# Performance work log

Measured on AMD Instinct MI355X. Metric: run time of the kernel, lower is better.

The kernel has to match this reference:

```python
import jax, jax.numpy as jnp
import numpy as np

LAYER_NORM_EPS = 1e-6
N_HEAD, D_MODEL, D_HEAD = 16, 1024, 64
QLEN, RLEN, BSZ = 2048, 2048, 2


def _rel_shift(x):
    # x: [T, C, b, n] -> Transformer-XL relative shift
    T, C = x.shape[0], x.shape[1]
    tail = x.shape[2:]
    zero_pad = jnp.zeros((T, 1) + tail, dtype=x.dtype)
    x_padded = jnp.concatenate([zero_pad, x], axis=1)          # [T, C+1, b, n]
    x_padded = x_padded.reshape((C + 1, T) + tail)             # [C+1, T, b, n]
    return x_padded[1:].reshape(x.shape)                       # [T, C, b, n]


def _layer_norm(x, gamma, beta):
    mu = jnp.mean(x, axis=-1, keepdims=True)
    var = jnp.mean(jnp.square(x - mu), axis=-1, keepdims=True)
    return (x - mu) * jax.lax.rsqrt(var + LAYER_NORM_EPS) * gamma + beta


def setup_inputs() -> dict:
    key = jax.random.key(0)
    ks = jax.random.split(key, 8)
    s_qkv = 1.0 / np.sqrt(D_MODEL)
    return {
        "h": jax.random.normal(ks[0], (QLEN, BSZ, D_MODEL), jnp.float32),
        "r": jax.random.normal(ks[1], (RLEN, D_MODEL), jnp.float32),
        "r_w_bias": jax.random.normal(ks[2], (N_HEAD, D_HEAD), jnp.float32) * 0.02,
        "r_r_bias": jax.random.normal(ks[3], (N_HEAD, D_HEAD), jnp.float32) * 0.02,
        "W_qkv": jax.random.normal(ks[4], (D_MODEL, 3 * N_HEAD * D_HEAD), jnp.float32) * s_qkv,
        "W_r": jax.random.normal(ks[5], (D_MODEL, N_HEAD * D_HEAD), jnp.float32) * s_qkv,
        "W_o": jax.random.normal(ks[6], (N_HEAD * D_HEAD, D_MODEL), jnp.float32) * s_qkv,
        "ln_gamma": jnp.ones((D_MODEL,), jnp.float32),
        "ln_beta": jnp.zeros((D_MODEL,), jnp.float32),
    }


def reference(h, r, r_w_bias, r_r_bias, W_qkv, W_r, W_o, ln_gamma, ln_beta):
    qlen, bsz = h.shape[0], h.shape[1]
    n_head, d_head = N_HEAD, D_HEAD
    scale = 1.0 / np.sqrt(d_head).astype(np.float32)

    w_heads = h @ W_qkv                                   # [q, b, 3*n*d]
    w_q, w_k, w_v = jnp.split(w_heads, 3, axis=-1)
    r_k = (r @ W_r).reshape(r.shape[0], n_head, d_head)    # [rlen, n, d]

    klen = w_k.shape[0]
    w_q = w_q.reshape(qlen, bsz, n_head, d_head)
    w_k = w_k.reshape(klen, bsz, n_head, d_head)
    w_v = w_v.reshape(klen, bsz, n_head, d_head)

    AC = jnp.einsum('ibnd,jbnd->ijbn', w_q + r_w_bias, w_k)
    BD = jnp.einsum('ibnd,jnd->ijbn', w_q + r_r_bias, r_k)
    BD = _rel_shift(BD)

    attn_score = (AC + BD) * scale                         # [q, k, b, n]
    attn_prob = jax.nn.softmax(attn_score, axis=1)

    attn_vec = jnp.einsum('ijbn,jbnd->ibnd', attn_prob, w_v)
    attn_vec = attn_vec.reshape(qlen, bsz, n_head * d_head)
    attn_out = attn_vec @ W_o                              # [q, b, d_model]

    # post-norm residual (pre_norm=False)
    return _layer_norm(h + attn_out, ln_gamma, ln_beta)
```

## Files before the change

### kernel.cpp

```cpp
#include <hip/hip_runtime.h>
#include <hip/hip_bf16.h>

typedef unsigned short u16;
typedef __attribute__((ext_vector_type(8))) short s16x8;
typedef __attribute__((ext_vector_type(8))) unsigned short u16x8;
typedef __attribute__((ext_vector_type(4))) float f32x4;

#define SEQ 2048
#define KEXP 0.18033688011112042f

__device__ __forceinline__ float bf2f(u16 x) {
  union { unsigned u; float f; } c; c.u = ((unsigned)x) << 16; return c.f;
}
__device__ __forceinline__ u16 f2bf(float f) {
  __hip_bfloat16 h = __float2bfloat16(f);
  return __builtin_bit_cast(u16, h);
}
__device__ __forceinline__ unsigned pack2(float a, float b) {
  return (unsigned)f2bf(a) | ((unsigned)f2bf(b) << 16);
}

__global__ __launch_bounds__(256) void k_cvt(const float* __restrict__ src,
                                             u16* __restrict__ dst, int n4) {
  int i = blockIdx.x * 256 + threadIdx.x;
  if (i >= n4) return;
  float4 v = ((const float4*)src)[i];
  ((ushort4*)dst)[i] = make_ushort4(f2bf(v.x), f2bf(v.y), f2bf(v.z), f2bf(v.w));
}

__global__ __launch_bounds__(256) void k_tcvt(const float* __restrict__ src,
                                              u16* __restrict__ dst, int R, int C) {
  __shared__ u16 T[64][72];
  int r0 = blockIdx.y * 64, c0 = blockIdx.x * 64;
  int tid = threadIdx.x;
#pragma unroll
  for (int p = 0; p < 4; ++p) {
    int f = p * 256 + tid;
    int r = f >> 4, cc = (f & 15) * 4;
    float4 v = *(const float4*)(src + (size_t)(r0 + r) * C + c0 + cc);
    T[r][cc + 0] = f2bf(v.x); T[r][cc + 1] = f2bf(v.y);
    T[r][cc + 2] = f2bf(v.z); T[r][cc + 3] = f2bf(v.w);
  }
  __syncthreads();
#pragma unroll
  for (int p = 0; p < 2; ++p) {
    int f = p * 256 + tid;
    int c = f >> 3, rr = (f & 7) * 8;
    u16x8 v;
#pragma unroll
    for (int e = 0; e < 8; ++e) v[e] = T[rr + e][c];
    *(u16x8*)(dst + (size_t)(c0 + c) * R + r0 + rr) = v;
  }
}

template <int RES>
__global__ __launch_bounds__(256) void k_gemm_bt(const u16* __restrict__ A,
                                                 const u16* __restrict__ Bt,
                                                 u16* __restrict__ Cb,
                                                 float* __restrict__ Cf,
                                                 const float* __restrict__ res,
                                                 int M, int N, int K) {
  __shared__ u16 As[128 * 72];
  __shared__ u16 Bs[128 * 72];
  const int tid = threadIdx.x;
  const int l = tid & 63, wv = tid >> 6;
  const int g = l >> 4, c16 = l & 15;
  const int m0 = blockIdx.x * 128, n0 = blockIdx.y * 128;
  const int wr = (wv >> 1) * 64, wc = (wv & 1) * 64;
  f32x4 acc[4][4] = {};
  for (int k0 = 0; k0 < K; k0 += 64) {
    __syncthreads();
#pragma unroll
    for (int p = 0; p < 4; ++p) {
      int f = p * 256 + tid;
      int row = f >> 3, kb = (f & 7) * 8;
      u16x8 va = *(const u16x8*)(A + (size_t)(m0 + row) * K + k0 + kb);
      u16x8 vb = *(const u16x8*)(Bt + (size_t)(n0 + row) * K + k0 + kb);
      *(u16x8*)&As[row * 72 + kb] = va;
      *(u16x8*)&Bs[row * 72 + kb] = vb;
    }
    __syncthreads();
#pragma unroll
    for (int ks = 0; ks < 2; ++ks) {
      s16x8 af[4], bf[4];
#pragma unroll
      for (int fr = 0; fr < 4; ++fr)
        af[fr] = *(const s16x8*)&As[(wr + fr * 16 + c16) * 72 + ks * 32 + g * 8];
#pragma unroll
      for (int fc = 0; fc < 4; ++fc)
        bf[fc] = *(const s16x8*)&Bs[(wc + fc * 16 + c16) * 72 + ks * 32 + g * 8];
#pragma unroll
      for (int fr = 0; fr < 4; ++fr)
#pragma unroll
        for (int fc = 0; fc < 4; ++fc)
          acc[fr][fc] = __builtin_amdgcn_mfma_f32_16x16x32_bf16(af[fr], bf[fc],
                                                                acc[fr][fc], 0, 0, 0);
    }
  }
#pragma unroll
  for (int fr = 0; fr < 4; ++fr)
#pragma unroll
    for (int fc = 0; fc < 4; ++fc)
#pragma unroll
      for (int reg = 0; reg < 4; ++reg) {
        int row = m0 + wr + fr * 16 + g * 4 + reg;
        int col = n0 + wc + fc * 16 + c16;
        float v = acc[fr][fc][reg];
        if (RES) Cf[(size_t)row * N + col] = v + res[(size_t)row * N + col];
        else     Cb[(size_t)row * N + col] = f2bf(v);
      }
}

__global__ __launch_bounds__(256) void k_vt(const u16* __restrict__ qkv,
                                            u16* __restrict__ vT) {
  __shared__ u16 T[64][72];
  const int tid = threadIdx.x;
  const int j0 = blockIdx.x * 64;
  const int n = blockIdx.y & 15, b = blockIdx.y >> 4;
#pragma unroll
  for (int p = 0; p < 2; ++p) {
    int f = p * 256 + tid;
    int r = f >> 3, cc = (f & 7) * 8;
    *(u16x8*)&T[r][cc] =
        *(const u16x8*)(qkv + ((size_t)((j0 + r) * 2 + b)) * 3072 + 2048 + n * 64 + cc);
  }
  __syncthreads();
#pragma unroll
  for (int p = 0; p < 2; ++p) {
    int f = p * 256 + tid;
    int d = f >> 3, jc = (f & 7) * 8;
    u16x8 v;
#pragma unroll
    for (int e = 0; e < 8; ++e) v[e] = T[jc + e][d];
    *(u16x8*)(vT + ((size_t)((b * 16 + n) * 64 + d)) * 2048 + j0 + jc) = v;
  }
}

__global__ __launch_bounds__(256) void k_attn(const u16* __restrict__ qkv,
                                              const u16* __restrict__ rk,
                                              const u16* __restrict__ vT,
                                              const float* __restrict__ rwb,
                                              const float* __restrict__ rrb,
                                              u16* __restrict__ av) {
  __shared__ u16 Kt[128][72];
  __shared__ u16 Vt[64][136];
  __shared__ u16 St[192][66];
  __shared__ u16 Pt[64][136];

  const int tid = threadIdx.x;
  const int l = tid & 63, wv = tid >> 6;
  const int g = l >> 4, c16 = l & 15;
  const int s = blockIdx.x;
  const int y = (s & 7) + 8 * (s >> 8);
  const int x = (s >> 3) & 31;
  const int i0 = x * 64;
  const int n = y & 15, b = y >> 4;
  const f32x4 zero4 = {0.f, 0.f, 0.f, 0.f};
  const s16x8 zero8 = {0, 0, 0, 0, 0, 0, 0, 0};

  s16x8 qw[2];
  {
    int i = i0 + wv * 16 + c16;
    const u16* src = qkv + ((size_t)(i * 2 + b)) * 3072 + n * 64;
#pragma unroll
    for (int ks = 0; ks < 2; ++ks) {
      int d0 = ks * 32 + g * 8;
      u16x8 raw = *(const u16x8*)(src + d0);
      u16x8 wq;
#pragma unroll
      for (int e = 0; e < 8; ++e)
        wq[e] = f2bf(bf2f(raw[e]) + rwb[n * 64 + d0 + e]);
      qw[ks] = __builtin_bit_cast(s16x8, wq);
    }
  }
  s16x8 qr_a[4][2];
#pragma unroll
  for (int rg = 0; rg < 4; ++rg) {
    int i = i0 + rg * 16 + c16;
    const u16* src = qkv + ((size_t)(i * 2 + b)) * 3072 + n * 64;
#pragma unroll
    for (int ks = 0; ks < 2; ++ks) {
      int d0 = ks * 32 + g * 8;
      u16x8 raw = *(const u16x8*)(src + d0);
      u16x8 wq;
#pragma unroll
      for (int e = 0; e < 8; ++e)
        wq[e] = f2bf(bf2f(raw[e]) + rrb[n * 64 + d0 + e]);
      qr_a[rg][ks] = __builtin_bit_cast(s16x8, wq);
    }
  }
  s16x8 q64[2];
  {
    bool valid = (c16 == 0) && (i0 + 64 < SEQ);
#pragma unroll
    for (int ks = 0; ks < 2; ++ks) q64[ks] = zero8;
    if (valid) {
      const u16* src = qkv + ((size_t)((i0 + 64) * 2 + b)) * 3072 + n * 64;
#pragma unroll
      for (int ks = 0; ks < 2; ++ks) {
        int d0 = ks * 32 + g * 8;
        u16x8 raw = *(const u16x8*)(src + d0);
        u16x8 wq;
#pragma unroll
        for (int e = 0; e < 8; ++e)
          wq[e] = f2bf(bf2f(raw[e]) + rrb[n * 64 + d0 + e]);
        q64[ks] = __builtin_bit_cast(s16x8, wq);
      }
    }
  }

  u16x8 kpre[4], vpre[4];
  s16x8 rpre[3][2];
  auto issue_loads = [&](int j0n) {
#pragma unroll
    for (int p = 0; p < 4; ++p) {
      int f = p * 256 + tid;
      kpre[p] = *(const u16x8*)(qkv + ((size_t)((j0n + (f >> 3)) * 2 + b)) * 3072 +
                                1024 + n * 64 + (f & 7) * 8);
    }
#pragma unroll
    for (int p = 0; p < 4; ++p) {
      int f = p * 256 + tid;
      vpre[p] = *(const u16x8*)(vT + ((size_t)((b * 16 + n) * 64 + (f >> 4))) * 2048 +
                                j0n + (f & 15) * 8);
    }
#pragma unroll
    for (int c3 = 0; c3 < 3; ++c3) {
      int w = (wv * 3 + c3) * 16 + c16;
      int u = j0n - i0 - 63 + w;
      int c = (u <= 0) ? (u + (SEQ - 1)) : (u - 2);
      const u16* p = rk + (size_t)(c < 0 ? 0 : c) * 1024 + n * 64;
      rpre[c3][0] = *(const s16x8*)(p + g * 8);
      rpre[c3][1] = *(const s16x8*)(p + 32 + g * 8);
      if (c < 0) { rpre[c3][0] = zero8; rpre[c3][1] = zero8; }
    }
  };

  float m_prev[4], l_sum[4];
  f32x4 o_acc[4];
#pragma unroll
  for (int r = 0; r < 4; ++r) { m_prev[r] = -1e30f; l_sum[r] = 0.f; o_acc[r] = zero4; }

  issue_loads(0);

  for (int it = 0; it < 16; ++it) {
    const int j0 = it * 128;
    const int cfthr = (64 + i0 - j0) >> 4;
    __syncthreads();

#pragma unroll
    for (int p = 0; p < 4; ++p) {
      int f = p * 256 + tid;
      *(u16x8*)&Kt[f >> 3][(f & 7) * 8] = kpre[p];
    }
#pragma unroll
    for (int p = 0; p < 4; ++p) {
      int f = p * 256 + tid;
      *(u16x8*)&Vt[f >> 4][(f & 15) * 8] = vpre[p];
    }

#pragma unroll
    for (int c3 = 0; c3 < 3; ++c3) {
      const int cfe = wv * 3 + c3;
      const bool du = (cfe >= cfthr);
      const int w = cfe * 16 + c16;
#pragma unroll
      for (int rg = 0; rg < 4; ++rg) {
        f32x4 qr = zero4;
        qr = __builtin_amdgcn_mfma_f32_16x16x32_bf16(qr_a[rg][0], rpre[c3][0], qr, 0, 0, 0);
        qr = __builtin_amdgcn_mfma_f32_16x16x32_bf16(qr_a[rg][1], rpre[c3][1], qr, 0, 0, 0);
        const int B = rg * 16 + g * 4;
        if (!du) {
          *(unsigned*)&St[w][B] = pack2(qr[0], qr[1]);
          *(unsigned*)&St[w][B + 2] = pack2(qr[2], qr[3]);
        } else if (B == 0) {
          *(unsigned*)&St[w][0] = pack2(qr[1], qr[2]);
          St[w][2] = f2bf(qr[3]);
        } else {
          St[w][B - 1] = f2bf(qr[0]);
          *(unsigned*)&St[w][B] = pack2(qr[1], qr[2]);
          St[w][B + 2] = f2bf(qr[3]);
        }
      }
      if (du) {
        f32x4 q64o = zero4;
        q64o = __builtin_amdgcn_mfma_f32_16x16x32_bf16(q64[0], rpre[c3][0], q64o, 0, 0, 0);
        q64o = __builtin_amdgcn_mfma_f32_16x16x32_bf16(q64[1], rpre[c3][1], q64o, 0, 0, 0);
        if (g == 0) St[w][63] = f2bf(q64o[0]);
      }
    }
    __syncthreads();

    f32x4 sc[8];
#pragma unroll
    for (int fj = 0; fj < 8; ++fj) sc[fj] = zero4;
#pragma unroll
    for (int ks = 0; ks < 2; ++ks)
#pragma unroll
      for (int fj = 0; fj < 8; ++fj) {
        s16x8 bf = *(const s16x8*)&Kt[fj * 16 + c16][ks * 32 + g * 8];
        sc[fj] = __builtin_amdgcn_mfma_f32_16x16x32_bf16(qw[ks], bf, sc[fj], 0, 0, 0);
      }

    {
      const char* Sbase = (const char*)&St[0][0] +
                          (c16 * 132 - (wv * 16 + g * 4) * 130 + 7926);
#pragma unroll
      for (int fj = 0; fj < 8; ++fj)
#pragma unroll
        for (int reg = 0; reg < 4; ++reg)
          sc[fj][reg] += bf2f(*(const u16*)(Sbase + fj * 2112 + (3 - reg) * 130));
    }

    float mt[4];
#pragma unroll
    for (int reg = 0; reg < 4; ++reg) {
      mt[reg] = sc[0][reg];
#pragma unroll
      for (int fj = 1; fj < 8; ++fj) mt[reg] = fmaxf(mt[reg], sc[fj][reg]);
    }
#pragma unroll
    for (int off = 1; off < 16; off <<= 1)
#pragma unroll
      for (int reg = 0; reg < 4; ++reg)
        mt[reg] = fmaxf(mt[reg], __shfl_xor(mt[reg], off, 16));
    float al[4], rs[4];
#pragma unroll
    for (int reg = 0; reg < 4; ++reg) {
      float mn = fmaxf(m_prev[reg], mt[reg]);
      al[reg] = __builtin_amdgcn_exp2f((m_prev[reg] - mn) * KEXP);
      m_prev[reg] = mn;
      rs[reg] = 0.f;
    }
#pragma unroll
    for (int fj = 0; fj < 8; ++fj)
#pragma unroll
      for (int reg = 0; reg < 4; ++reg) {
        float p = __builtin_amdgcn_exp2f((sc[fj][reg] - m_prev[reg]) * KEXP);
        rs[reg] += p;
        Pt[wv * 16 + g * 4 + reg][fj * 16 + c16] = f2bf(p);
      }
#pragma unroll
    for (int off = 1; off < 16; off <<= 1)
#pragma unroll
      for (int reg = 0; reg < 4; ++reg)
        rs[reg] += __shfl_xor(rs[reg], off, 16);
#pragma unroll
    for (int reg = 0; reg < 4; ++reg)
      l_sum[reg] = l_sum[reg] * al[reg] + rs[reg];
#pragma unroll
    for (int fd = 0; fd < 4; ++fd)
#pragma unroll
      for (int reg = 0; reg < 4; ++reg)
        o_acc[fd][reg] *= al[reg];

    if (it < 15) issue_loads(j0 + 128);

#pragma unroll
    for (int ks = 0; ks < 4; ++ks) {
      s16x8 pa = *(const s16x8*)&Pt[wv * 16 + c16][ks * 32 + g * 8];
#pragma unroll
      for (int fd = 0; fd < 4; ++fd) {
        s16x8 vb = *(const s16x8*)&Vt[fd * 16 + c16][ks * 32 + g * 8];
        o_acc[fd] = __builtin_amdgcn_mfma_f32_16x16x32_bf16(pa, vb, o_acc[fd], 0, 0, 0);
      }
    }
  }

#pragma unroll
  for (int reg = 0; reg < 4; ++reg) {
    float inv = 1.0f / l_sum[reg];
    int i = i0 + wv * 16 + g * 4 + reg;
    u16* dst = av + ((size_t)(i * 2 + b)) * 1024 + n * 64;
#pragma unroll
    for (int fd = 0; fd < 4; ++fd)
      dst[fd * 16 + c16] = f2bf(o_acc[fd][reg] * inv);
  }
}

__global__ __launch_bounds__(256) void k_ln(const float* __restrict__ tmp,
                                            const float* __restrict__ gamma,
                                            const float* __restrict__ beta,
                                            float* __restrict__ out) {
  __shared__ float r1[4], r2[4];
  const int row = blockIdx.x, tid = threadIdx.x;
  const float* x = tmp + (size_t)row * 1024;
  float4 v = *(const float4*)(x + tid * 4);
  float s1 = v.x + v.y + v.z + v.w;
  float s2 = v.x * v.x + v.y * v.y + v.z * v.z + v.w * v.w;
#pragma unroll
  for (int off = 1; off < 64; off <<= 1) {
    s1 += __shfl_xor(s1, off, 64);
    s2 += __shfl_xor(s2, off, 64);
  }
  if ((tid & 63) == 0) { r1[tid >> 6] = s1; r2[tid >> 6] = s2; }
  __syncthreads();
  s1 = r1[0] + r1[1] + r1[2] + r1[3];
  s2 = r2[0] + r2[1] + r2[2] + r2[3];
  float mu = s1 * (1.f / 1024.f);
  float var = s2 * (1.f / 1024.f) - mu * mu;
  float rstd = rsqrtf(var + 1e-6f);
  float4 gm = *(const float4*)(gamma + tid * 4);
  float4 bt = *(const float4*)(beta + tid * 4);
  float4 o;
  o.x = (v.x - mu) * rstd * gm.x + bt.x;
  o.y = (v.y - mu) * rstd * gm.y + bt.y;
  o.z = (v.z - mu) * rstd * gm.z + bt.z;
  o.w = (v.w - mu) * rstd * gm.w + bt.w;
  *(float4*)(out + (size_t)row * 1024 + tid * 4) = o;
}

extern "C" void kernel_launch(void* const* d_in, const int* in_sizes, int n_in,
                              void* d_out, int out_size, void* d_ws, size_t ws_size,
                              hipStream_t stream) {
  const float* h    = (const float*)d_in[0];
  const float* r    = (const float*)d_in[1];
  const float* rwb  = (const float*)d_in[2];
  const float* rrb  = (const float*)d_in[3];
  const float* Wqkv = (const float*)d_in[4];
  const float* Wr   = (const float*)d_in[5];
  const float* Wo   = (const float*)d_in[6];
  const float* gam  = (const float*)d_in[7];
  const float* bet  = (const float*)d_in[8];
  float* out = (float*)d_out;

  u16* hb     = (u16*)d_ws;
  u16* Wqkv_t = hb + (size_t)4096 * 1024;
  u16* Wr_t   = Wqkv_t + (size_t)3072 * 1024;
  u16* Wo_t   = Wr_t + (size_t)1024 * 1024;
  u16* rb     = Wo_t + (size_t)1024 * 1024;
  u16* qkv    = rb + (size_t)2048 * 1024;
  u16* rk     = qkv + (size_t)4096 * 3072;
  u16* vT     = rk + (size_t)2048 * 1024;
  u16* av     = vT + (size_t)2 * 16 * 64 * 2048;
  float* tmp  = (float*)(av + (size_t)4096 * 1024);

  k_cvt<<<4096, 256, 0, stream>>>(h, hb, 4096 * 1024 / 4);
  k_cvt<<<2048, 256, 0, stream>>>(r, rb, 2048 * 1024 / 4);
  k_tcvt<<<dim3(48, 16), 256, 0, stream>>>(Wqkv, Wqkv_t, 1024, 3072);
  k_tcvt<<<dim3(16, 16), 256, 0, stream>>>(Wr, Wr_t, 1024, 1024);
  k_tcvt<<<dim3(16, 16), 256, 0, stream>>>(Wo, Wo_t, 1024, 1024);
  k_gemm_bt<0><<<dim3(32, 24), 256, 0, stream>>>(hb, Wqkv_t, qkv, nullptr, nullptr,
                                                 4096, 3072, 1024);
  k_gemm_bt<0><<<dim3(16, 8), 256, 0, stream>>>(rb, Wr_t, rk, nullptr, nullptr,
                                                2048, 1024, 1024);
  k_vt<<<dim3(32, 32), 256, 0, stream>>>(qkv, vT);
  k_attn<<<1024, 256, 0, stream>>>(qkv, rk, vT, rwb, rrb, av);
  k_gemm_bt<1><<<dim3(32, 8), 256, 0, stream>>>(av, Wo_t, nullptr, tmp, h,
                                                4096, 1024, 1024);
  k_ln<<<4096, 256, 0, stream>>>(tmp, gam, bet, out);
}
```

Before: 279.3 us.

## Transpose attention score MFMA so softmax reductions stay per-lane

```diff
diff --git a/kernel.cpp b/kernel.cpp
--- a/kernel.cpp
+++ b/kernel.cpp
@@ -144,8 +144,8 @@
                                               u16* __restrict__ av) {
   __shared__ u16 Kt[128][72];
   __shared__ u16 Vt[64][136];
-  __shared__ u16 St[192][66];
-  __shared__ u16 Pt[64][136];
+  __shared__ u16 St2[64 * 200];
+  __shared__ u16 Pt[4][16][136];
 
   const int tid = threadIdx.x;
   const int l = tid & 63, wv = tid >> 6;
@@ -155,6 +155,7 @@
   const int x = (s >> 3) & 31;
   const int i0 = x * 64;
   const int n = y & 15, b = y >> 4;
+  const int ii = wv * 16 + c16;
   const f32x4 zero4 = {0.f, 0.f, 0.f, 0.f};
   const s16x8 zero8 = {0, 0, 0, 0, 0, 0, 0, 0};
 
@@ -173,29 +174,14 @@
       qw[ks] = __builtin_bit_cast(s16x8, wq);
     }
   }
-  s16x8 qr_a[4][2];
-#pragma unroll
-  for (int rg = 0; rg < 4; ++rg) {
-    int i = i0 + rg * 16 + c16;
-    const u16* src = qkv + ((size_t)(i * 2 + b)) * 3072 + n * 64;
-#pragma unroll
-    for (int ks = 0; ks < 2; ++ks) {
-      int d0 = ks * 32 + g * 8;
-      u16x8 raw = *(const u16x8*)(src + d0);
-      u16x8 wq;
-#pragma unroll
-      for (int e = 0; e < 8; ++e)
-        wq[e] = f2bf(bf2f(raw[e]) + rrb[n * 64 + d0 + e]);
-      qr_a[rg][ks] = __builtin_bit_cast(s16x8, wq);
-    }
-  }
-  s16x8 q64[2];
-  {
-    bool valid = (c16 == 0) && (i0 + 64 < SEQ);
-#pragma unroll
-    for (int ks = 0; ks < 2; ++ks) q64[ks] = zero8;
-    if (valid) {
-      const u16* src = qkv + ((size_t)((i0 + 64) * 2 + b)) * 3072 + n * 64;
+  s16x8 qr_b[4][2], qr_b1[4][2];
+#pragma unroll
+  for (int rb = 0; rb < 4; ++rb) {
+#pragma unroll
+    for (int sh = 0; sh < 2; ++sh) {
+      int i = i0 + rb * 16 + c16 + sh;
+      if (i > SEQ - 1) i = SEQ - 1;
+      const u16* src = qkv + ((size_t)(i * 2 + b)) * 3072 + n * 64;
 #pragma unroll
       for (int ks = 0; ks < 2; ++ks) {
         int d0 = ks * 32 + g * 8;
@@ -204,7 +190,8 @@
 #pragma unroll
         for (int e = 0; e < 8; ++e)
           wq[e] = f2bf(bf2f(raw[e]) + rrb[n * 64 + d0 + e]);
-        q64[ks] = __builtin_bit_cast(s16x8, wq);
+        if (sh == 0) qr_b[rb][ks] = __builtin_bit_cast(s16x8, wq);
+        else         qr_b1[rb][ks] = __builtin_bit_cast(s16x8, wq);
       }
     }
   }
@@ -236,16 +223,16 @@
     }
   };
 
-  float m_prev[4], l_sum[4];
+  float m_prev = -1e30f, l_sum = 0.f;
   f32x4 o_acc[4];
 #pragma unroll
-  for (int r = 0; r < 4; ++r) { m_prev[r] = -1e30f; l_sum[r] = 0.f; o_acc[r] = zero4; }
+  for (int r = 0; r < 4; ++r) o_acc[r] = zero4;
 
   issue_loads(0);
 
   for (int it = 0; it < 16; ++it) {
     const int j0 = it * 128;
-    const int cfthr = (64 + i0 - j0) >> 4;
+    const int wbthr = (64 + i0 - j0) >> 4;
     __syncthreads();
 
 #pragma unroll
@@ -261,32 +248,19 @@
 
 #pragma unroll
     for (int c3 = 0; c3 < 3; ++c3) {
-      const int cfe = wv * 3 + c3;
-      const bool du = (cfe >= cfthr);
-      const int w = cfe * 16 + c16;
-#pragma unroll
-      for (int rg = 0; rg < 4; ++rg) {
-        f32x4 qr = zero4;
-        qr = __builtin_amdgcn_mfma_f32_16x16x32_bf16(qr_a[rg][0], rpre[c3][0], qr, 0, 0, 0);
-        qr = __builtin_amdgcn_mfma_f32_16x16x32_bf16(qr_a[rg][1], rpre[c3][1], qr, 0, 0, 0);
-        const int B = rg * 16 + g * 4;
-        if (!du) {
-          *(unsigned*)&St[w][B] = pack2(qr[0], qr[1]);
-          *(unsigned*)&St[w][B + 2] = pack2(qr[2], qr[3]);
-        } else if (B == 0) {
-          *(unsigned*)&St[w][0] = pack2(qr[1], qr[2]);
-          St[w][2] = f2bf(qr[3]);
-        } else {
-          St[w][B - 1] = f2bf(qr[0]);
-          *(unsigned*)&St[w][B] = pack2(qr[1], qr[2]);
-          St[w][B + 2] = f2bf(qr[3]);
-        }
-      }
-      if (du) {
-        f32x4 q64o = zero4;
-        q64o = __builtin_amdgcn_mfma_f32_16x16x32_bf16(q64[0], rpre[c3][0], q64o, 0, 0, 0);
-        q64o = __builtin_amdgcn_mfma_f32_16x16x32_bf16(q64[1], rpre[c3][1], q64o, 0, 0, 0);
-        if (g == 0) St[w][63] = f2bf(q64o[0]);
+      const int wb = wv * 3 + c3;
+      const bool du = (wb >= wbthr);
+#pragma unroll
+      for (int rb = 0; rb < 4; ++rb) {
+        s16x8 b0 = du ? qr_b1[rb][0] : qr_b[rb][0];
+        s16x8 b1 = du ? qr_b1[rb][1] : qr_b[rb][1];
+        f32x4 q = zero4;
+        q = __builtin_amdgcn_mfma_f32_16x16x32_bf16(rpre[c3][0], b0, q, 0, 0, 0);
+        q = __builtin_amdgcn_mfma_f32_16x16x32_bf16(rpre[c3][1], b1, q, 0, 0, 0);
+        uint2 pk;
+        pk.x = pack2(q[0], q[1]);
+        pk.y = pack2(q[2], q[3]);
+        *(uint2*)&St2[(rb * 16 + c16) * 200 + wb * 16 + g * 4] = pk;
       }
     }
     __syncthreads();
@@ -298,67 +272,67 @@
     for (int ks = 0; ks < 2; ++ks)
 #pragma unroll
       for (int fj = 0; fj < 8; ++fj) {
-        s16x8 bf = *(const s16x8*)&Kt[fj * 16 + c16][ks * 32 + g * 8];
-        sc[fj] = __builtin_amdgcn_mfma_f32_16x16x32_bf16(qw[ks], bf, sc[fj], 0, 0, 0);
+        s16x8 kf = *(const s16x8*)&Kt[fj * 16 + c16][ks * 32 + g * 8];
+        sc[fj] = __builtin_amdgcn_mfma_f32_16x16x32_bf16(kf, qw[ks], sc[fj], 0, 0, 0);
       }
 
     {
-      const char* Sbase = (const char*)&St[0][0] +
-                          (c16 * 132 - (wv * 16 + g * 4) * 130 + 7926);
+      const u16* Sb = &St2[ii * 199 + g * 4 + 63];
 #pragma unroll
       for (int fj = 0; fj < 8; ++fj)
 #pragma unroll
         for (int reg = 0; reg < 4; ++reg)
-          sc[fj][reg] += bf2f(*(const u16*)(Sbase + fj * 2112 + (3 - reg) * 130));
-    }
-
-    float mt[4];
-#pragma unroll
-    for (int reg = 0; reg < 4; ++reg) {
-      mt[reg] = sc[0][reg];
-#pragma unroll
-      for (int fj = 1; fj < 8; ++fj) mt[reg] = fmaxf(mt[reg], sc[fj][reg]);
-    }
-#pragma unroll
-    for (int off = 1; off < 16; off <<= 1)
+          sc[fj][reg] += bf2f(Sb[fj * 16 + reg]);
+    }
+
+    float mt = sc[0][0];
+#pragma unroll
+    for (int fj = 0; fj < 8; ++fj)
 #pragma unroll
       for (int reg = 0; reg < 4; ++reg)
-        mt[reg] = fmaxf(mt[reg], __shfl_xor(mt[reg], off, 16));
-    float al[4], rs[4];
-#pragma unroll
-    for (int reg = 0; reg < 4; ++reg) {
-      float mn = fmaxf(m_prev[reg], mt[reg]);
-      al[reg] = __builtin_amdgcn_exp2f((m_prev[reg] - mn) * KEXP);
-      m_prev[reg] = mn;
-      rs[reg] = 0.f;
-    }
+        mt = fmaxf(mt, sc[fj][reg]);
+    mt = fmaxf(mt, __shfl_xor(mt, 16));
+    mt = fmaxf(mt, __shfl_xor(mt, 32));
+    float mn = fmaxf(m_prev, mt);
+    float al = __builtin_amdgcn_exp2f((m_prev - mn) * KEXP);
+    m_prev = mn;
+    float mk = mn * KEXP;
+    float rs = 0.f;
 #pragma unroll
     for (int fj = 0; fj < 8; ++fj)
 #pragma unroll
       for (int reg = 0; reg < 4; ++reg) {
-        float p = __builtin_amdgcn_exp2f((sc[fj][reg] - m_prev[reg]) * KEXP);
-        rs[reg] += p;
-        Pt[wv * 16 + g * 4 + reg][fj * 16 + c16] = f2bf(p);
-      }
-#pragma unroll
-    for (int off = 1; off < 16; off <<= 1)
+        float p = __builtin_amdgcn_exp2f(fmaf(sc[fj][reg], KEXP, -mk));
+        rs += p;
+        sc[fj][reg] = p;
+      }
+    rs += __shfl_xor(rs, 16);
+    rs += __shfl_xor(rs, 32);
+    l_sum = l_sum * al + rs;
+
+    float al_t[4];
+#pragma unroll
+    for (int reg = 0; reg < 4; ++reg)
+      al_t[reg] = __shfl(al, g * 4 + reg, 64);
+#pragma unroll
+    for (int fd = 0; fd < 4; ++fd)
 #pragma unroll
       for (int reg = 0; reg < 4; ++reg)
-        rs[reg] += __shfl_xor(rs[reg], off, 16);
-#pragma unroll
-    for (int reg = 0; reg < 4; ++reg)
-      l_sum[reg] = l_sum[reg] * al[reg] + rs[reg];
-#pragma unroll
-    for (int fd = 0; fd < 4; ++fd)
-#pragma unroll
-      for (int reg = 0; reg < 4; ++reg)
-        o_acc[fd][reg] *= al[reg];
+        o_acc[fd][reg] *= al_t[reg];
+
+#pragma unroll
+    for (int fj = 0; fj < 8; ++fj) {
+      uint2 pk;
+      pk.x = pack2(sc[fj][0], sc[fj][1]);
+      pk.y = pack2(sc[fj][2], sc[fj][3]);
+      *(uint2*)&Pt[wv][c16][fj * 16 + g * 4] = pk;
+    }
 
     if (it < 15) issue_loads(j0 + 128);
 
 #pragma unroll
     for (int ks = 0; ks < 4; ++ks) {
-      s16x8 pa = *(const s16x8*)&Pt[wv * 16 + c16][ks * 32 + g * 8];
+      s16x8 pa = *(const s16x8*)&Pt[wv][c16][ks * 32 + g * 8];
 #pragma unroll
       for (int fd = 0; fd < 4; ++fd) {
         s16x8 vb = *(const s16x8*)&Vt[fd * 16 + c16][ks * 32 + g * 8];
@@ -367,14 +341,18 @@
     }
   }
 
+  float linv = 1.0f / l_sum;
+  float linv_t[4];
+#pragma unroll
+  for (int reg = 0; reg < 4; ++reg)
+    linv_t[reg] = __shfl(linv, g * 4 + reg, 64);
 #pragma unroll
   for (int reg = 0; reg < 4; ++reg) {
-    float inv = 1.0f / l_sum[reg];
     int i = i0 + wv * 16 + g * 4 + reg;
     u16* dst = av + ((size_t)(i * 2 + b)) * 1024 + n * 64;
 #pragma unroll
     for (int fd = 0; fd < 4; ++fd)
-      dst[fd * 16 + c16] = f2bf(o_acc[fd][reg] * inv);
+      dst[fd * 16 + c16] = f2bf(o_acc[fd][reg] * linv_t[reg]);
   }
 }
 
```

Result: slower. 394.8 us (+41.4%).
